# Kernel optimization log

Measured on AMD Instinct MI355X. Metric: run time of the kernel, lower is better.

## Reference

```python
import jax, jax.numpy as jnp
import numpy as np
from jax import lax

DIM = 48
HEADS = 8
B, H, W = 4, 256, 256
EPS = 1e-12  # torch F.normalize eps


def conv1x1(x, w):
    # x: [b,c,h,w], w: [out,c] (1x1 conv, no bias)
    return jnp.einsum('bchw,oc->bohw', x, w)


def dwconv3x3(x, w):
    # depthwise 3x3, padding 1; w: [C,1,3,3]
    return lax.conv_general_dilated(
        x, w, window_strides=(1, 1), padding=((1, 1), (1, 1)),
        dimension_numbers=('NCHW', 'OIHW', 'NCHW'),
        feature_group_count=x.shape[1])


def setup_inputs() -> dict:
    key = jax.random.key(0)
    ks = jax.random.split(key, 8)
    s = 0.05
    return {
        'fea_0': jax.random.normal(ks[0], (B, DIM, H, W), jnp.float32),
        'fea_1': jax.random.normal(ks[1], (B, DIM, H, W), jnp.float32),
        'qk_w': jax.random.normal(ks[2], (2 * DIM, DIM), jnp.float32) * s,
        'qk_dw_w': jax.random.normal(ks[3], (2 * DIM, 1, 3, 3), jnp.float32) * s,
        'v_w': jax.random.normal(ks[4], (DIM, DIM), jnp.float32) * s,
        'v_dw_w': jax.random.normal(ks[5], (DIM, 1, 3, 3), jnp.float32) * s,
        'proj_w': jax.random.normal(ks[6], (DIM, DIM), jnp.float32) * s,
        'temperature': jnp.ones((HEADS, 1, 1), jnp.float32),
    }


def reference(fea_0, fea_1, qk_w, qk_dw_w, v_w, v_dw_w, proj_w, temperature):
    b, c, h, w = fea_0.shape
    ch = c // HEADS  # channels per head
    qk = dwconv3x3(conv1x1(fea_0, qk_w), qk_dw_w)
    q, k = jnp.split(qk, 2, axis=1)
    v = dwconv3x3(conv1x1(fea_1, v_w), v_dw_w)
    # [b, head, c_per_head, h*w]
    q = q.reshape(b, HEADS, ch, h * w)
    k = k.reshape(b, HEADS, ch, h * w)
    v = v.reshape(b, HEADS, ch, h * w)
    q = q / jnp.maximum(jnp.linalg.norm(q, axis=-1, keepdims=True), EPS)
    k = k / jnp.maximum(jnp.linalg.norm(k, axis=-1, keepdims=True), EPS)
    attn = jnp.einsum('bhcn,bhdn->bhcd', q, k) * temperature[None]
    attn = jax.nn.softmax(attn, axis=-1)
    out = jnp.einsum('bhcd,bhdn->bhcn', attn, v)
    out = out.reshape(b, c, h, w)
    return conv1x1(out, proj_w)
```

## Files before the change

kernel.cpp:

```cpp
#include <hip/hip_runtime.h>
#include <cstddef>

#define IMG 256
#define HW 65536
#define NB 4
#define NHEADS 8
#define TW 32
#define TH 8
#define HAW 34
#define HAH 10
#define HP2 (HAW*HAH)
#define NTILE 256
#define XSP 28

typedef short bf16x8 __attribute__((ext_vector_type(8)));
typedef float f32x4 __attribute__((ext_vector_type(4)));
typedef float f32x16 __attribute__((ext_vector_type(16)));

__device__ __forceinline__ unsigned short f2bf(float f) {
    unsigned int x = __float_as_uint(f);
    unsigned int r = (x + 0x7fffu + ((x >> 16) & 1u)) >> 16;
    return (unsigned short)r;
}

__device__ __forceinline__ int xcd_map(int bid, int nwg) {
    const int q = nwg >> 3, r = nwg & 7;
    const int x = bid & 7, i = bid >> 3;
    return (x < r ? x * (q + 1) : r * (q + 1) + (x - r) * q) + i;
}

__global__ __launch_bounds__(256) void prep_qcw_kernel(
    const float* __restrict__ qk_w, const float* __restrict__ qk_dw,
    unsigned short* __restrict__ qcwb) {
    const int idx = blockIdx.x * 256 + threadIdx.x;
    const int e16 = idx & 15;
    const int slot = (idx >> 4) & 127;
    const int tk = idx >> 11;
    const int ks = tk % 3;
    const int head = slot >> 4, sub = slot & 15;
    float v = 0.f;
    if (sub < 12) {
        const int row = (sub < 6) ? (head * 6 + sub) : (48 + head * 6 + (sub - 6));
        v = qk_dw[row * 9 + tk / 3] * qk_w[row * 48 + ks * 16 + e16];
    }
    qcwb[idx] = f2bf(v);
}

__global__ __launch_bounds__(256, 4) void fused_qk_stats_kernel(
    const float* __restrict__ fea0, const unsigned short* __restrict__ qcwb,
    float* __restrict__ stats) {
    __shared__ __align__(16) unsigned short xs[HP2][XSP];
    __shared__ __align__(16) unsigned short sg[4][16][72];
    __shared__ float sacc[384];

    const int tid = threadIdx.x;
    const int b = blockIdx.y;
    const int mp = xcd_map(blockIdx.x, 2 * NTILE);
    const int tile = mp >> 1, p = mp & 1;
    const int tx = tile & 7, ty = tile >> 3;
    const float* fb = fea0 + (size_t)b * 48 * HW;

    for (int i = tid; i < 384; i += 256) sacc[i] = 0.f;

    const int wave = tid >> 6, lane = tid & 63;
    const int l31 = lane & 31, lhi = lane >> 5;
    const int m = wave & 1, g = wave >> 1;

    f32x16 C[4];
#pragma unroll
    for (int nf = 0; nf < 4; ++nf)
#pragma unroll
        for (int r = 0; r < 16; ++r) C[nf][r] = 0.f;

#pragma unroll
    for (int ks = 0; ks < 3; ++ks) {
        __syncthreads();
        for (int hp = tid; hp < HP2; hp += 256) {
            const int hx = hp % HAW, hy = hp / HAW;
            const int gx = tx * TW + hx - 1, gy = ty * TH + hy - 1;
            const bool inb = ((unsigned)gx < (unsigned)IMG) && ((unsigned)gy < (unsigned)IMG);
            const int pix = inb ? (gy * IMG + gx) : 0;
            bf16x8 t0, t1;
#pragma unroll
            for (int c = 0; c < 8; ++c) {
                t0[c] = (short)f2bf(inb ? fb[(size_t)(ks * 16 + c) * HW + pix] : 0.f);
                t1[c] = (short)f2bf(inb ? fb[(size_t)(ks * 16 + 8 + c) * HW + pix] : 0.f);
            }
            *(bf16x8*)&xs[hp][0] = t0;
            *(bf16x8*)&xs[hp][8] = t1;
        }
        __syncthreads();

#pragma unroll
        for (int tap = 0; tap < 9; ++tap) {
            const int dy = tap / 3, dx = tap % 3;
            const bf16x8 a = *(const bf16x8*)&qcwb[(size_t)((tap * 3 + ks) * 128 + p * 64 + m * 32 + l31) * 16 + lhi * 8];
#pragma unroll
            for (int nf = 0; nf < 4; ++nf) {
                const int hrow = (4 * g + nf + dy) * HAW + l31 + dx;
                const bf16x8 bb = *(const bf16x8*)&xs[hrow][lhi * 8];
                C[nf] = __builtin_amdgcn_mfma_f32_32x32x16_bf16(a, bb, C[nf], 0, 0, 0);
            }
        }
    }

    const int fr = lane & 15, fg = lane >> 4;

#define DO_STATS(CA, CB, hbase)                                                   \
    {                                                                             \
        _Pragma("unroll")                                                         \
        for (int hh = 0; hh < 2; ++hh) {                                          \
            _Pragma("unroll")                                                     \
            for (int rq = 0; rq < 2; ++rq) {                                      \
                if (!(rq && lhi)) {                                               \
                    _Pragma("unroll")                                             \
                    for (int j = 0; j < 4; ++j) {                                 \
                        const int sub = j + 8 * rq + 4 * lhi;                     \
                        sg[wave][sub][l31] = f2bf(CA[hh * 8 + rq * 4 + j]);       \
                        sg[wave][sub][32 + l31] = f2bf(CB[hh * 8 + rq * 4 + j]);  \
                    }                                                             \
                }                                                                 \
            }                                                                     \
            asm volatile("s_waitcnt lgkmcnt(0)" ::: "memory");                    \
            __builtin_amdgcn_sched_barrier(0);                                    \
            const bf16x8 a0 = *(const bf16x8*)&sg[wave][fr][fg * 8];              \
            const bf16x8 a1 = *(const bf16x8*)&sg[wave][fr][32 + fg * 8];         \
            asm volatile("s_waitcnt lgkmcnt(0)" ::: "memory");                    \
            __builtin_amdgcn_sched_barrier(0);                                    \
            f32x4 c4 = {0.f, 0.f, 0.f, 0.f};                                      \
            c4 = __builtin_amdgcn_mfma_f32_16x16x32_bf16(a0, a0, c4, 0, 0, 0);    \
            c4 = __builtin_amdgcn_mfma_f32_16x16x32_bf16(a1, a1, c4, 0, 0, 0);    \
            const int h = (hbase) + hh;                                           \
            _Pragma("unroll")                                                     \
            for (int r = 0; r < 4; ++r) {                                         \
                const int crow = fg * 4 + r;                                      \
                const float vv = c4[r];                                           \
                if (crow < 6) {                                                   \
                    if (fr == crow) atomicAdd(&sacc[h * 6 + crow], vv);           \
                    else if (fr >= 6 && fr < 12)                                  \
                        atomicAdd(&sacc[96 + h * 36 + crow * 6 + (fr - 6)], vv);  \
                } else if (crow < 12 && fr == crow) {                             \
                    atomicAdd(&sacc[48 + h * 6 + (crow - 6)], vv);                \
                }                                                                 \
            }                                                                     \
        }                                                                         \
    }

    DO_STATS(C[0], C[1], p * 4 + m * 2)
    DO_STATS(C[2], C[3], p * 4 + m * 2)
#undef DO_STATS

    __syncthreads();
    for (int i = tid; i < 192; i += 256) {
        int idx;
        if (i < 24) idx = p * 24 + i;
        else if (i < 48) idx = 48 + p * 24 + (i - 24);
        else idx = 96 + p * 144 + (i - 48);
        atomicAdd(&stats[b * 384 + idx], sacc[idx]);
    }
}

__global__ __launch_bounds__(256) void softmax_w2_cw_kernel(
    const float* __restrict__ stats, const float* __restrict__ proj_w,
    const float* __restrict__ temperature, const float* __restrict__ v_w,
    const float* __restrict__ v_dw, unsigned short* __restrict__ cwb) {
    const int b = blockIdx.x;
    const int tid = threadIdx.x;
    __shared__ float attn[NHEADS * 36];
    __shared__ float W2s[48 * 48];
    const float* sb = stats + b * 384;

    if (tid < 48) {
        const int h = tid / 6, cc = tid % 6;
        float nq = fmaxf(sqrtf(sb[tid]), 1e-12f);
        const float tmp = temperature[h];
        float lo[6];
#pragma unroll
        for (int d = 0; d < 6; ++d) {
            const float nk = fmaxf(sqrtf(sb[48 + h * 6 + d]), 1e-12f);
            lo[d] = sb[96 + h * 36 + cc * 6 + d] / (nq * nk) * tmp;
        }
        float m = lo[0];
#pragma unroll
        for (int d = 1; d < 6; ++d) m = fmaxf(m, lo[d]);
        float s = 0.f;
#pragma unroll
        for (int d = 0; d < 6; ++d) { lo[d] = expf(lo[d] - m); s += lo[d]; }
        const float inv = 1.f / s;
#pragma unroll
        for (int d = 0; d < 6; ++d) attn[h * 36 + cc * 6 + d] = lo[d] * inv;
    }
    __syncthreads();

    for (int idx = tid; idx < 48 * 48; idx += 256) {
        const int c = idx / 48, dg = idx % 48;
        const int h = dg / 6, hd = dg % 6;
        float s = 0.f;
#pragma unroll
        for (int cc = 0; cc < 6; ++cc)
            s = fmaf(proj_w[c * 48 + h * 6 + cc], attn[h * 36 + cc * 6 + hd], s);
        W2s[idx] = s;
    }
    __syncthreads();

    unsigned short* cb = cwb + (size_t)b * 27648;
    for (int pp = 0; pp < 9; ++pp) {
        const int pair = pp * 256 + tid;
        const int c = pair / 48, e = pair % 48;
        float acc[9];
#pragma unroll
        for (int t = 0; t < 9; ++t) acc[t] = 0.f;
        for (int d = 0; d < 48; ++d) {
            const float wv = W2s[c * 48 + d] * v_w[d * 48 + e];
#pragma unroll
            for (int t = 0; t < 9; ++t)
                acc[t] = fmaf(wv, v_dw[d * 9 + t], acc[t]);
        }
#pragma unroll
        for (int t = 0; t < 9; ++t)
            cb[(size_t)((t * 3 + (e >> 4)) * 64 + c) * 16 + (e & 15)] = f2bf(acc[t]);
    }
    for (int i = tid; i < 6912; i += 256) {
        const int e16 = i & 15;
        const int cp = 48 + ((i >> 4) & 15);
        const int tk = i >> 8;
        cb[(size_t)(tk * 64 + cp) * 16 + e16] = 0;
    }
}

__global__ __launch_bounds__(256, 4) void conv3x3_out_kernel(
    const float* __restrict__ fea1, const unsigned short* __restrict__ cwb,
    float* __restrict__ out) {
    __shared__ __align__(16) unsigned short xs[HP2][XSP];

    const int tid = threadIdx.x;
    const int b = blockIdx.y;
    const int tile = xcd_map(blockIdx.x, NTILE);
    const int tx = tile & 7, ty = tile >> 3;
    const float* fb = fea1 + (size_t)b * 48 * HW;
    const unsigned short* cb = cwb + (size_t)b * 27648;

    const int wave = tid >> 6, lane = tid & 63;
    const int l31 = lane & 31, lhi = lane >> 5;
    const int m = wave & 1, g = wave >> 1;

    f32x16 C[4];
#pragma unroll
    for (int nf = 0; nf < 4; ++nf)
#pragma unroll
        for (int r = 0; r < 16; ++r) C[nf][r] = 0.f;

#pragma unroll
    for (int ks = 0; ks < 3; ++ks) {
        __syncthreads();
        for (int hp = tid; hp < HP2; hp += 256) {
            const int hx = hp % HAW, hy = hp / HAW;
            const int gx = tx * TW + hx - 1, gy = ty * TH + hy - 1;
            const bool inb = ((unsigned)gx < (unsigned)IMG) && ((unsigned)gy < (unsigned)IMG);
            const int pix = inb ? (gy * IMG + gx) : 0;
            bf16x8 t0, t1;
#pragma unroll
            for (int c = 0; c < 8; ++c) {
                t0[c] = (short)f2bf(inb ? fb[(size_t)(ks * 16 + c) * HW + pix] : 0.f);
                t1[c] = (short)f2bf(inb ? fb[(size_t)(ks * 16 + 8 + c) * HW + pix] : 0.f);
            }
            *(bf16x8*)&xs[hp][0] = t0;
            *(bf16x8*)&xs[hp][8] = t1;
        }
        __syncthreads();

#pragma unroll
        for (int tap = 0; tap < 9; ++tap) {
            const int dy = tap / 3, dx = tap % 3;
            const bf16x8 a = *(const bf16x8*)&cb[(size_t)((tap * 3 + ks) * 64 + m * 32 + l31) * 16 + lhi * 8];
#pragma unroll
            for (int nf = 0; nf < 4; ++nf) {
                const int hrow = (4 * g + nf + dy) * HAW + l31 + dx;
                const bf16x8 bb = *(const bf16x8*)&xs[hrow][lhi * 8];
                C[nf] = __builtin_amdgcn_mfma_f32_32x32x16_bf16(a, bb, C[nf], 0, 0, 0);
            }
        }
    }

    float* ob = out + (size_t)b * 48 * HW;
#pragma unroll
    for (int nf = 0; nf < 4; ++nf) {
        const int gpx = (ty * TH + 4 * g + nf) * IMG + tx * TW + l31;
#pragma unroll
        for (int r = 0; r < 16; ++r) {
            const int och = m * 32 + (r & 3) + 8 * (r >> 2) + 4 * lhi;
            if (m == 0 || r < 8) ob[(size_t)och * HW + gpx] = C[nf][r];
        }
    }
}

extern "C" void kernel_launch(void* const* d_in, const int* in_sizes, int n_in,
                              void* d_out, int out_size, void* d_ws, size_t ws_size,
                              hipStream_t stream) {
    const float* fea0 = (const float*)d_in[0];
    const float* fea1 = (const float*)d_in[1];
    const float* qk_w = (const float*)d_in[2];
    const float* qk_dw = (const float*)d_in[3];
    const float* v_w = (const float*)d_in[4];
    const float* v_dw = (const float*)d_in[5];
    const float* proj_w = (const float*)d_in[6];
    const float* temperature = (const float*)d_in[7];
    float* out = (float*)d_out;

    char* ws = (char*)d_ws;
    float* stats = (float*)ws;
    unsigned short* cwb = (unsigned short*)(ws + 8192);
    unsigned short* qcwb = (unsigned short*)(ws + 8192 + 221184);

    hipMemsetAsync(stats, 0, (size_t)NB * 384 * sizeof(float), stream);

    prep_qcw_kernel<<<216, 256, 0, stream>>>(qk_w, qk_dw, qcwb);
    fused_qk_stats_kernel<<<dim3(2 * NTILE, NB), 256, 0, stream>>>(fea0, qcwb, stats);
    softmax_w2_cw_kernel<<<NB, 256, 0, stream>>>(stats, proj_w, temperature, v_w, v_dw, cwb);
    conv3x3_out_kernel<<<dim3(NTILE, NB), 256, 0, stream>>>(fea1, cwb, out);
}
```

Before: 119.6 us.

## Stage all 48 input channels in LDS once and merge qk-stats block pair

Both conv kernels now load the full 48-channel halo tile into shared memory in a single pass, instead of three 16-channel passes with barriers between them. The weight layout becomes tap-major with 48 contiguous channels, and the loop is reordered to tap-outer, ks-inner. The qk-stats kernel merges the two per-tile blocks (the p halves) into one 512-thread block, so fea0 is read once per tile, and it reuses the LDS buffer for the stats scratch. The cost is a doubled LDS footprint (XSP 56), which lowers occupancy, and a larger block that may limit how many blocks fit per CU.

```diff
diff --git a/kernel.cpp b/kernel.cpp
--- a/kernel.cpp
+++ b/kernel.cpp
@@ -11,7 +11,7 @@
 #define HAH 10
 #define HP2 (HAW*HAH)
 #define NTILE 256
-#define XSP 28
+#define XSP 56
 
 typedef short bf16x8 __attribute__((ext_vector_type(8)));
 typedef float f32x4 __attribute__((ext_vector_type(4)));
@@ -33,38 +33,55 @@
     const float* __restrict__ qk_w, const float* __restrict__ qk_dw,
     unsigned short* __restrict__ qcwb) {
     const int idx = blockIdx.x * 256 + threadIdx.x;
-    const int e16 = idx & 15;
-    const int slot = (idx >> 4) & 127;
-    const int tk = idx >> 11;
-    const int ks = tk % 3;
+    const int e = idx % 48;
+    const int slot = (idx / 48) & 127;
+    const int tap = idx / (48 * 128);
     const int head = slot >> 4, sub = slot & 15;
     float v = 0.f;
     if (sub < 12) {
         const int row = (sub < 6) ? (head * 6 + sub) : (48 + head * 6 + (sub - 6));
-        v = qk_dw[row * 9 + tk / 3] * qk_w[row * 48 + ks * 16 + e16];
+        v = qk_dw[row * 9 + tap] * qk_w[row * 48 + e];
     }
     qcwb[idx] = f2bf(v);
 }
 
-__global__ __launch_bounds__(256, 4) void fused_qk_stats_kernel(
+__global__ __launch_bounds__(512, 4) void fused_qk_stats_kernel(
     const float* __restrict__ fea0, const unsigned short* __restrict__ qcwb,
     float* __restrict__ stats) {
     __shared__ __align__(16) unsigned short xs[HP2][XSP];
-    __shared__ __align__(16) unsigned short sg[4][16][72];
     __shared__ float sacc[384];
 
     const int tid = threadIdx.x;
     const int b = blockIdx.y;
-    const int mp = xcd_map(blockIdx.x, 2 * NTILE);
-    const int tile = mp >> 1, p = mp & 1;
+    const int tile = xcd_map(blockIdx.x, NTILE);
     const int tx = tile & 7, ty = tile >> 3;
     const float* fb = fea0 + (size_t)b * 48 * HW;
 
-    for (int i = tid; i < 384; i += 256) sacc[i] = 0.f;
+    for (int i = tid; i < 384; i += 512) sacc[i] = 0.f;
+
+    for (int i = tid; i < 2 * HP2; i += 512) {
+        const int hp = i >> 1, half = i & 1;
+        const int hx = hp % HAW, hy = hp / HAW;
+        const int gx = tx * TW + hx - 1, gy = ty * TH + hy - 1;
+        const bool inb = ((unsigned)gx < (unsigned)IMG) && ((unsigned)gy < (unsigned)IMG);
+        const int pix = inb ? (gy * IMG + gx) : 0;
+        const int ch0 = half * 24;
+        unsigned int w[12];
+#pragma unroll
+        for (int c = 0; c < 12; ++c) {
+            const float lo = inb ? fb[(size_t)(ch0 + 2 * c) * HW + pix] : 0.f;
+            const float hi = inb ? fb[(size_t)(ch0 + 2 * c + 1) * HW + pix] : 0.f;
+            w[c] = (unsigned)f2bf(lo) | ((unsigned)f2bf(hi) << 16);
+        }
+#pragma unroll
+        for (int c = 0; c < 12; ++c)
+            *(unsigned int*)&xs[hp][ch0 + 2 * c] = w[c];
+    }
+    __syncthreads();
 
     const int wave = tid >> 6, lane = tid & 63;
     const int l31 = lane & 31, lhi = lane >> 5;
-    const int m = wave & 1, g = wave >> 1;
+    const int p = wave >> 2, m = (wave >> 1) & 1, g = wave & 1;
 
     f32x16 C[4];
 #pragma unroll
@@ -72,38 +89,29 @@
 #pragma unroll
         for (int r = 0; r < 16; ++r) C[nf][r] = 0.f;
 
-#pragma unroll
-    for (int ks = 0; ks < 3; ++ks) {
-        __syncthreads();
-        for (int hp = tid; hp < HP2; hp += 256) {
-            const int hx = hp % HAW, hy = hp / HAW;
-            const int gx = tx * TW + hx - 1, gy = ty * TH + hy - 1;
-            const bool inb = ((unsigned)gx < (unsigned)IMG) && ((unsigned)gy < (unsigned)IMG);
-            const int pix = inb ? (gy * IMG + gx) : 0;
-            bf16x8 t0, t1;
-#pragma unroll
-            for (int c = 0; c < 8; ++c) {
-                t0[c] = (short)f2bf(inb ? fb[(size_t)(ks * 16 + c) * HW + pix] : 0.f);
-                t1[c] = (short)f2bf(inb ? fb[(size_t)(ks * 16 + 8 + c) * HW + pix] : 0.f);
-            }
-            *(bf16x8*)&xs[hp][0] = t0;
-            *(bf16x8*)&xs[hp][8] = t1;
-        }
-        __syncthreads();
-
-#pragma unroll
-        for (int tap = 0; tap < 9; ++tap) {
-            const int dy = tap / 3, dx = tap % 3;
-            const bf16x8 a = *(const bf16x8*)&qcwb[(size_t)((tap * 3 + ks) * 128 + p * 64 + m * 32 + l31) * 16 + lhi * 8];
+    const unsigned short* abase =
+        qcwb + ((size_t)(p * 64 + m * 32 + l31) * 48 + lhi * 8);
+
+#pragma unroll
+    for (int tap = 0; tap < 9; ++tap) {
+        const int dy = tap / 3, dx = tap % 3;
+        const bf16x8 A0 = *(const bf16x8*)(abase + (size_t)tap * 6144);
+        const bf16x8 A1 = *(const bf16x8*)(abase + (size_t)tap * 6144 + 16);
+        const bf16x8 A2 = *(const bf16x8*)(abase + (size_t)tap * 6144 + 32);
+        const int rbase = (4 * g + dy) * HAW + l31 + dx;
+#pragma unroll
+        for (int ks = 0; ks < 3; ++ks) {
+            const bf16x8 a = (ks == 0) ? A0 : ((ks == 1) ? A1 : A2);
 #pragma unroll
             for (int nf = 0; nf < 4; ++nf) {
-                const int hrow = (4 * g + nf + dy) * HAW + l31 + dx;
-                const bf16x8 bb = *(const bf16x8*)&xs[hrow][lhi * 8];
+                const bf16x8 bb = *(const bf16x8*)&xs[rbase + nf * HAW][ks * 16 + lhi * 8];
                 C[nf] = __builtin_amdgcn_mfma_f32_32x32x16_bf16(a, bb, C[nf], 0, 0, 0);
             }
         }
     }
 
+    __syncthreads();
+    auto sg = reinterpret_cast<unsigned short (*)[16][72]>(&xs[0][0]);
     const int fr = lane & 15, fg = lane >> 4;
 
 #define DO_STATS(CA, CB, hbase)                                                   \
@@ -151,13 +159,7 @@
 #undef DO_STATS
 
     __syncthreads();
-    for (int i = tid; i < 192; i += 256) {
-        int idx;
-        if (i < 24) idx = p * 24 + i;
-        else if (i < 48) idx = 48 + p * 24 + (i - 24);
-        else idx = 96 + p * 144 + (i - 48);
-        atomicAdd(&stats[b * 384 + idx], sacc[idx]);
-    }
+    for (int i = tid; i < 384; i += 512) atomicAdd(&stats[b * 384 + i], sacc[i]);
 }
 
 __global__ __launch_bounds__(256) void softmax_w2_cw_kernel(
@@ -218,13 +220,13 @@
         }
 #pragma unroll
         for (int t = 0; t < 9; ++t)
-            cb[(size_t)((t * 3 + (e >> 4)) * 64 + c) * 16 + (e & 15)] = f2bf(acc[t]);
+            cb[(size_t)(t * 64 + c) * 48 + e] = f2bf(acc[t]);
     }
     for (int i = tid; i < 6912; i += 256) {
-        const int e16 = i & 15;
-        const int cp = 48 + ((i >> 4) & 15);
-        const int tk = i >> 8;
-        cb[(size_t)(tk * 64 + cp) * 16 + e16] = 0;
+        const int e = i % 48;
+        const int cp = 48 + ((i / 48) & 15);
+        const int t = i / 768;
+        cb[(size_t)(t * 64 + cp) * 48 + e] = 0;
     }
 }
 
@@ -240,6 +242,26 @@
     const float* fb = fea1 + (size_t)b * 48 * HW;
     const unsigned short* cb = cwb + (size_t)b * 27648;
 
+    for (int i = tid; i < 2 * HP2; i += 256) {
+        const int hp = i >> 1, half = i & 1;
+        const int hx = hp % HAW, hy = hp / HAW;
+        const int gx = tx * TW + hx - 1, gy = ty * TH + hy - 1;
+        const bool inb = ((unsigned)gx < (unsigned)IMG) && ((unsigned)gy < (unsigned)IMG);
+        const int pix = inb ? (gy * IMG + gx) : 0;
+        const int ch0 = half * 24;
+        unsigned int w[12];
+#pragma unroll
+        for (int c = 0; c < 12; ++c) {
+            const float lo = inb ? fb[(size_t)(ch0 + 2 * c) * HW + pix] : 0.f;
+            const float hi = inb ? fb[(size_t)(ch0 + 2 * c + 1) * HW + pix] : 0.f;
+            w[c] = (unsigned)f2bf(lo) | ((unsigned)f2bf(hi) << 16);
+        }
+#pragma unroll
+        for (int c = 0; c < 12; ++c)
+            *(unsigned int*)&xs[hp][ch0 + 2 * c] = w[c];
+    }
+    __syncthreads();
+
     const int wave = tid >> 6, lane = tid & 63;
     const int l31 = lane & 31, lhi = lane >> 5;
     const int m = wave & 1, g = wave >> 1;
@@ -250,33 +272,21 @@
 #pragma unroll
         for (int r = 0; r < 16; ++r) C[nf][r] = 0.f;
 
-#pragma unroll
-    for (int ks = 0; ks < 3; ++ks) {
-        __syncthreads();
-        for (int hp = tid; hp < HP2; hp += 256) {
-            const int hx = hp % HAW, hy = hp / HAW;
-            const int gx = tx * TW + hx - 1, gy = ty * TH + hy - 1;
-            const bool inb = ((unsigned)gx < (unsigned)IMG) && ((unsigned)gy < (unsigned)IMG);
-            const int pix = inb ? (gy * IMG + gx) : 0;
-            bf16x8 t0, t1;
-#pragma unroll
-            for (int c = 0; c < 8; ++c) {
-                t0[c] = (short)f2bf(inb ? fb[(size_t)(ks * 16 + c) * HW + pix] : 0.f);
-                t1[c] = (short)f2bf(inb ? fb[(size_t)(ks * 16 + 8 + c) * HW + pix] : 0.f);
-            }
-            *(bf16x8*)&xs[hp][0] = t0;
-            *(bf16x8*)&xs[hp][8] = t1;
-        }
-        __syncthreads();
-
-#pragma unroll
-        for (int tap = 0; tap < 9; ++tap) {
-            const int dy = tap / 3, dx = tap % 3;
-            const bf16x8 a = *(const bf16x8*)&cb[(size_t)((tap * 3 + ks) * 64 + m * 32 + l31) * 16 + lhi * 8];
+    const unsigned short* abase = cb + ((size_t)(m * 32 + l31) * 48 + lhi * 8);
+
+#pragma unroll
+    for (int tap = 0; tap < 9; ++tap) {
+        const int dy = tap / 3, dx = tap % 3;
+        const bf16x8 A0 = *(const bf16x8*)(abase + (size_t)tap * 3072);
+        const bf16x8 A1 = *(const bf16x8*)(abase + (size_t)tap * 3072 + 16);
+        const bf16x8 A2 = *(const bf16x8*)(abase + (size_t)tap * 3072 + 32);
+        const int rbase = (4 * g + dy) * HAW + l31 + dx;
+#pragma unroll
+        for (int ks = 0; ks < 3; ++ks) {
+            const bf16x8 a = (ks == 0) ? A0 : ((ks == 1) ? A1 : A2);
 #pragma unroll
             for (int nf = 0; nf < 4; ++nf) {
-                const int hrow = (4 * g + nf + dy) * HAW + l31 + dx;
-                const bf16x8 bb = *(const bf16x8*)&xs[hrow][lhi * 8];
+                const bf16x8 bb = *(const bf16x8*)&xs[rbase + nf * HAW][ks * 16 + lhi * 8];
                 C[nf] = __builtin_amdgcn_mfma_f32_32x32x16_bf16(a, bb, C[nf], 0, 0, 0);
             }
         }
@@ -315,7 +325,7 @@
     hipMemsetAsync(stats, 0, (size_t)NB * 384 * sizeof(float), stream);
 
     prep_qcw_kernel<<<216, 256, 0, stream>>>(qk_w, qk_dw, qcwb);
-    fused_qk_stats_kernel<<<dim3(2 * NTILE, NB), 256, 0, stream>>>(fea0, qcwb, stats);
+    fused_qk_stats_kernel<<<dim3(NTILE, NB), 512, 0, stream>>>(fea0, qcwb, stats);
     softmax_w2_cw_kernel<<<NB, 256, 0, stream>>>(stats, proj_w, temperature, v_w, v_dw, cwb);
     conv3x3_out_kernel<<<dim3(NTILE, NB), 256, 0, stream>>>(fea1, cwb, out);
 }
```

Result: slower. 202.5 us (+69.4%).
